# Kernel optimization log

Measured on AMD Instinct MI355X. Metric: run time of the kernel, lower is better.

Reference implementation:

```python
import jax, jax.numpy as jnp
import numpy as np

B, S, D, U = 32, 4096, 512, 128

def setup_inputs() -> dict:
    key = jax.random.key(0)
    k1, k2, k3, k4, k5 = jax.random.split(key, 5)
    query = jax.random.normal(k1, (B, D), dtype=jnp.float32)
    values = jax.random.normal(k2, (B, S, D), dtype=jnp.float32)
    s = 1.0 / np.sqrt(D)
    W1 = jax.random.normal(k3, (D, U), dtype=jnp.float32) * s
    W2 = jax.random.normal(k4, (D, U), dtype=jnp.float32) * s
    V = jax.random.normal(k5, (U, 1), dtype=jnp.float32) * (1.0 / np.sqrt(U))
    b1 = jnp.zeros((U,), dtype=jnp.float32)
    b2 = jnp.zeros((U,), dtype=jnp.float32)
    bv = jnp.zeros((1,), dtype=jnp.float32)
    return {"query": query, "values": values, "W1": W1, "b1": b1,
            "W2": W2, "b2": b2, "V": V, "bv": bv}

def reference(query, values, W1, b1, W2, b2, V, bv):
    # query: [B, D] -> [B, 1, U]; values: [B, S, D] -> [B, S, U]
    q_proj = (query @ W1 + b1)[:, None, :]                  # [B, 1, U]
    v_proj = jnp.einsum('bsd,du->bsu', values, W2) + b2      # [B, S, U]
    score = jnp.tanh(q_proj + v_proj) @ V + bv               # [B, S, 1]
    attention_weights = jax.nn.softmax(score, axis=1)        # [B, S, 1]
    context_vector = jnp.sum(attention_weights * values, axis=1)  # [B, D]
    return context_vector, attention_weights
```

## Files before the change

### kernel.cpp

```cpp
#include <hip/hip_runtime.h>
#include <math.h>

#define NB 32
#define NS 4096
#define ND 512
#define NU 128
#define RR 32
#define ASTR 520
#define BSTR 40

typedef __bf16 bf16x8 __attribute__((ext_vector_type(8)));
typedef unsigned short u16x8 __attribute__((ext_vector_type(8)));
typedef float f32x4 __attribute__((ext_vector_type(4)));

union FragCvt { u16x8 u; bf16x8 b; };

__device__ inline unsigned short f2bf(float x) {
  union { float f; unsigned u; } v; v.f = x;
  return (unsigned short)((v.u + 0x7FFFu + ((v.u >> 16) & 1u)) >> 16);
}
__device__ inline float bf2f(unsigned int bits16) {
  union { unsigned u; float f; } v; v.u = bits16 << 16;
  return v.f;
}

__global__ void prep_qb(const float* __restrict__ q, const float* __restrict__ W1,
                        const float* __restrict__ b1, const float* __restrict__ b2,
                        float* __restrict__ qb) {
  int idx = blockIdx.x * 256 + threadIdx.x;
  int b = idx >> 7, u = idx & 127;
  float s = b1[u] + b2[u];
  const float* qr = q + b * ND;
  for (int d = 0; d < ND; ++d) s += qr[d] * W1[d * NU + u];
  qb[idx] = s;
}

__global__ void prep_w2t(const float* __restrict__ W2, unsigned short* __restrict__ w2t) {
  int idx = blockIdx.x * 256 + threadIdx.x;
  int u = idx >> 9, d = idx & 511;
  w2t[idx] = f2bf(W2[d * NU + u]);
}

__global__ __launch_bounds__(256, 3) void fused_attn(
    const float* __restrict__ values,
    const float* __restrict__ qb,
    const unsigned short* __restrict__ w2t,
    const float* __restrict__ V,
    const float* __restrict__ bvp,
    float* __restrict__ wout,
    float* __restrict__ Cacc,
    float* __restrict__ Lacc)
{
  __shared__ unsigned short Alds[RR * ASTR];
  __shared__ unsigned short Blds[NU * BSTR];
  __shared__ float sbuf[4][16];
  __shared__ float wlds[RR];

  const int tid = threadIdx.x;
  const int b = blockIdx.x >> 7;
  const int chunk = blockIdx.x & 127;
  const int s0 = chunk * RR;

  const float* vbase = values + ((size_t)b * NS + s0) * ND;
  #pragma unroll
  for (int i = 0; i < 16; ++i) {
    int f = tid + 256 * i;
    int row = f >> 7;
    int c4 = f & 127;
    float4 v = *(const float4*)(vbase + row * ND + c4 * 4);
    ushort4 pk;
    pk.x = f2bf(v.x); pk.y = f2bf(v.y); pk.z = f2bf(v.z); pk.w = f2bf(v.w);
    *(ushort4*)(&Alds[row * ASTR + c4 * 4]) = pk;
  }

  const int wave = tid >> 6, lane = tid & 63;
  const int quad = lane >> 4, lidx = lane & 15;
  const int mtile = wave & 1;
  const int nbase = (wave >> 1) * 64;

  f32x4 acc[4] = {{0.f,0.f,0.f,0.f},{0.f,0.f,0.f,0.f},{0.f,0.f,0.f,0.f},{0.f,0.f,0.f,0.f}};

  const int bu = tid >> 1, bh = tid & 1;
  for (int kt = 0; kt < 16; ++kt) {
    __syncthreads();
    {
      const unsigned short* src = w2t + bu * ND + kt * 32 + bh * 16;
      u16x8 p0 = *(const u16x8*)(src);
      u16x8 p1 = *(const u16x8*)(src + 8);
      *(u16x8*)(&Blds[bu * BSTR + bh * 16])     = p0;
      *(u16x8*)(&Blds[bu * BSTR + bh * 16 + 8]) = p1;
    }
    __syncthreads();
    FragCvt af; af.u = *(const u16x8*)(&Alds[(mtile * 16 + lidx) * ASTR + kt * 32 + quad * 8]);
    #pragma unroll
    for (int nt = 0; nt < 4; ++nt) {
      FragCvt bf; bf.u = *(const u16x8*)(&Blds[(nbase + nt * 16 + lidx) * BSTR + quad * 8]);
      acc[nt] = __builtin_amdgcn_mfma_f32_16x16x32_bf16(af.b, bf.b, acc[nt], 0, 0, 0);
    }
  }

  float part[4] = {0.f, 0.f, 0.f, 0.f};
  #pragma unroll
  for (int nt = 0; nt < 4; ++nt) {
    int col = nbase + nt * 16 + lidx;
    float qv = qb[b * NU + col];
    float vv = V[col];
    #pragma unroll
    for (int r = 0; r < 4; ++r) {
      float t = tanhf(acc[nt][r] + qv);
      part[r] += t * vv;
    }
  }
  #pragma unroll
  for (int m = 1; m <= 8; m <<= 1) {
    #pragma unroll
    for (int r = 0; r < 4; ++r) part[r] += __shfl_xor(part[r], m, 64);
  }
  if (lidx == 0) {
    #pragma unroll
    for (int r = 0; r < 4; ++r) sbuf[wave][quad * 4 + r] = part[r];
  }
  __syncthreads();

  if (tid < 32) {
    int mt = tid >> 4, rr = tid & 15;
    float s = sbuf[mt][rr] + sbuf[mt + 2][rr];
    float e = expf(s + *bvp);
    wout[(size_t)b * NS + s0 + tid] = e;
    wlds[tid] = e;
    float es = e;
    #pragma unroll
    for (int m = 1; m <= 16; m <<= 1) es += __shfl_xor(es, m, 64);
    if (tid == 0) atomicAdd(Lacc + b, es);
  }
  __syncthreads();

  int d0 = tid * 2;
  float c0 = 0.f, c1 = 0.f;
  for (int r = 0; r < RR; ++r) {
    float w = wlds[r];
    unsigned int pk = *(const unsigned int*)(&Alds[r * ASTR + d0]);
    c0 += w * bf2f(pk & 0xFFFFu);
    c1 += w * bf2f(pk >> 16);
  }
  atomicAdd(Cacc + b * ND + d0, c0);
  atomicAdd(Cacc + b * ND + d0 + 1, c1);
}

__global__ void finalize(const float* __restrict__ Cacc, const float* __restrict__ Lacc,
                         float* __restrict__ out) {
  int idx = blockIdx.x * 256 + threadIdx.x;
  if (idx < NB * ND) {
    int b = idx >> 9;
    out[idx] = Cacc[idx] / Lacc[b];
  } else {
    int j = idx - NB * ND;
    int b = j >> 12;
    out[idx] = out[idx] / Lacc[b];
  }
}

extern "C" void kernel_launch(void* const* d_in, const int* in_sizes, int n_in,
                              void* d_out, int out_size, void* d_ws, size_t ws_size,
                              hipStream_t stream) {
  const float* query  = (const float*)d_in[0];
  const float* values = (const float*)d_in[1];
  const float* W1     = (const float*)d_in[2];
  const float* b1     = (const float*)d_in[3];
  const float* W2     = (const float*)d_in[4];
  const float* b2     = (const float*)d_in[5];
  const float* V      = (const float*)d_in[6];
  const float* bv     = (const float*)d_in[7];
  float* out = (float*)d_out;

  char* ws = (char*)d_ws;
  float* Cacc = (float*)ws;
  float* Lacc = (float*)(ws + 65536);
  float* qb   = (float*)(ws + 66048);
  unsigned short* w2t = (unsigned short*)(ws + 66048 + 16384);

  hipMemsetAsync(ws, 0, 66048, stream);

  prep_qb <<<16, 256, 0, stream>>>(query, W1, b1, b2, qb);
  prep_w2t<<<256, 256, 0, stream>>>(W2, w2t);
  fused_attn<<<NB * (NS / RR), 256, 0, stream>>>(values, qb, w2t, V, bv,
                                                 out + NB * ND, Cacc, Lacc);
  finalize<<<(NB * ND + NB * NS) / 256, 256, 0, stream>>>(Cacc, Lacc, out);
}
```

Before: 443.5 us.

## Restructure fused attention: direct global fragments, split-K waves, per-chunk context partials

The main kernel now uses 512 threads. Each wave loads its W2 fragments straight from global memory into registers and converts value rows from fp32 to bf16 in registers, so the LDS staging and the per-k-step barriers are gone. The K dimension is split across wave pairs and the partial sums are combined through LDS. The context sum re-reads values in fp32 from global (likely L2-resident) and writes per-chunk partials instead of issuing atomics, and finalize reduces those partials. The two prep kernels are merged into one launch and the memset shrinks. In exchange, values are read twice from memory/cache and the workspace grows to 8 MB of partials.

```diff
diff --git a/kernel.cpp b/kernel.cpp
--- a/kernel.cpp
+++ b/kernel.cpp
@@ -1,4 +1,5 @@
 #include <hip/hip_runtime.h>
+#include <hip/hip_bf16.h>
 #include <math.h>
 
 #define NB 32
@@ -6,125 +7,145 @@
 #define ND 512
 #define NU 128
 #define RR 32
-#define ASTR 520
-#define BSTR 40
+#define NCHUNK (NS / RR)
 
 typedef __bf16 bf16x8 __attribute__((ext_vector_type(8)));
 typedef unsigned short u16x8 __attribute__((ext_vector_type(8)));
 typedef float f32x4 __attribute__((ext_vector_type(4)));
-
 union FragCvt { u16x8 u; bf16x8 b; };
 
 __device__ inline unsigned short f2bf(float x) {
   union { float f; unsigned u; } v; v.f = x;
   return (unsigned short)((v.u + 0x7FFFu + ((v.u >> 16) & 1u)) >> 16);
 }
-__device__ inline float bf2f(unsigned int bits16) {
-  union { unsigned u; float f; } v; v.u = bits16 << 16;
-  return v.f;
-}
-
-__global__ void prep_qb(const float* __restrict__ q, const float* __restrict__ W1,
-                        const float* __restrict__ b1, const float* __restrict__ b2,
-                        float* __restrict__ qb) {
-  int idx = blockIdx.x * 256 + threadIdx.x;
-  int b = idx >> 7, u = idx & 127;
-  float s = b1[u] + b2[u];
-  const float* qr = q + b * ND;
-  for (int d = 0; d < ND; ++d) s += qr[d] * W1[d * NU + u];
-  qb[idx] = s;
-}
-
-__global__ void prep_w2t(const float* __restrict__ W2, unsigned short* __restrict__ w2t) {
-  int idx = blockIdx.x * 256 + threadIdx.x;
-  int u = idx >> 9, d = idx & 511;
-  w2t[idx] = f2bf(W2[d * NU + u]);
-}
-
-__global__ __launch_bounds__(256, 3) void fused_attn(
+
+__device__ inline u16x8 pack8(float4 a, float4 b) {
+  u16x8 r;
+  r[0] = f2bf(a.x); r[1] = f2bf(a.y); r[2] = f2bf(a.z); r[3] = f2bf(a.w);
+  r[4] = f2bf(b.x); r[5] = f2bf(b.y); r[6] = f2bf(b.z); r[7] = f2bf(b.w);
+  return r;
+}
+
+__global__ void prep(const float* __restrict__ q, const float* __restrict__ W1,
+                     const float* __restrict__ b1, const float* __restrict__ b2,
+                     const float* __restrict__ W2,
+                     float* __restrict__ qb, unsigned short* __restrict__ w2t) {
+  if (blockIdx.x < 16) {
+    int idx = blockIdx.x * 256 + threadIdx.x;
+    int b = idx >> 7, u = idx & 127;
+    float s = b1[u] + b2[u];
+    const float* qr = q + b * ND;
+    #pragma unroll 8
+    for (int d = 0; d < ND; ++d) s += qr[d] * W1[d * NU + u];
+    qb[idx] = s;
+  } else {
+    int idx = (blockIdx.x - 16) * 256 + threadIdx.x;
+    int u = idx >> 9, d = idx & 511;
+    w2t[idx] = f2bf(W2[d * NU + u]);
+  }
+}
+
+__global__ __launch_bounds__(512, 4) void fused_attn(
     const float* __restrict__ values,
     const float* __restrict__ qb,
     const unsigned short* __restrict__ w2t,
     const float* __restrict__ V,
     const float* __restrict__ bvp,
     float* __restrict__ wout,
-    float* __restrict__ Cacc,
+    float* __restrict__ Cpart,
     float* __restrict__ Lacc)
 {
-  __shared__ unsigned short Alds[RR * ASTR];
-  __shared__ unsigned short Blds[NU * BSTR];
-  __shared__ float sbuf[4][16];
-  __shared__ float wlds[RR];
+  __shared__ float cbuf[4][16][64];
+  __shared__ float sbuf[4][32];
+  __shared__ float wlds[32];
 
   const int tid = threadIdx.x;
   const int b = blockIdx.x >> 7;
   const int chunk = blockIdx.x & 127;
   const int s0 = chunk * RR;
-
-  const float* vbase = values + ((size_t)b * NS + s0) * ND;
-  #pragma unroll
-  for (int i = 0; i < 16; ++i) {
-    int f = tid + 256 * i;
-    int row = f >> 7;
-    int c4 = f & 127;
-    float4 v = *(const float4*)(vbase + row * ND + c4 * 4);
-    ushort4 pk;
-    pk.x = f2bf(v.x); pk.y = f2bf(v.y); pk.z = f2bf(v.z); pk.w = f2bf(v.w);
-    *(ushort4*)(&Alds[row * ASTR + c4 * 4]) = pk;
-  }
-
   const int wave = tid >> 6, lane = tid & 63;
   const int quad = lane >> 4, lidx = lane & 15;
-  const int mtile = wave & 1;
-  const int nbase = (wave >> 1) * 64;
-
-  f32x4 acc[4] = {{0.f,0.f,0.f,0.f},{0.f,0.f,0.f,0.f},{0.f,0.f,0.f,0.f},{0.f,0.f,0.f,0.f}};
-
-  const int bu = tid >> 1, bh = tid & 1;
-  for (int kt = 0; kt < 16; ++kt) {
-    __syncthreads();
-    {
-      const unsigned short* src = w2t + bu * ND + kt * 32 + bh * 16;
-      u16x8 p0 = *(const u16x8*)(src);
-      u16x8 p1 = *(const u16x8*)(src + 8);
-      *(u16x8*)(&Blds[bu * BSTR + bh * 16])     = p0;
-      *(u16x8*)(&Blds[bu * BSTR + bh * 16 + 8]) = p1;
-    }
-    __syncthreads();
-    FragCvt af; af.u = *(const u16x8*)(&Alds[(mtile * 16 + lidx) * ASTR + kt * 32 + quad * 8]);
-    #pragma unroll
-    for (int nt = 0; nt < 4; ++nt) {
-      FragCvt bf; bf.u = *(const u16x8*)(&Blds[(nbase + nt * 16 + lidx) * BSTR + quad * 8]);
-      acc[nt] = __builtin_amdgcn_mfma_f32_16x16x32_bf16(af.b, bf.b, acc[nt], 0, 0, 0);
-    }
-  }
-
-  float part[4] = {0.f, 0.f, 0.f, 0.f};
+  const int khalf = wave & 1, ng = wave >> 1;
+
+  const float* vbase = values + ((size_t)b * NS + s0) * ND;
+
+  FragCvt bfr[2][8];
   #pragma unroll
-  for (int nt = 0; nt < 4; ++nt) {
-    int col = nbase + nt * 16 + lidx;
-    float qv = qb[b * NU + col];
-    float vv = V[col];
-    #pragma unroll
-    for (int r = 0; r < 4; ++r) {
-      float t = tanhf(acc[nt][r] + qv);
-      part[r] += t * vv;
-    }
-  }
+  for (int nt = 0; nt < 2; ++nt) {
+    const int u = ng * 32 + nt * 16 + lidx;
+    #pragma unroll
+    for (int k8 = 0; k8 < 8; ++k8)
+      bfr[nt][k8].u = *(const u16x8*)(w2t + u * ND + (khalf * 8 + k8) * 32 + quad * 8);
+  }
+
+  f32x4 acc[2][2];
   #pragma unroll
-  for (int m = 1; m <= 8; m <<= 1) {
-    #pragma unroll
-    for (int r = 0; r < 4; ++r) part[r] += __shfl_xor(part[r], m, 64);
-  }
-  if (lidx == 0) {
-    #pragma unroll
-    for (int r = 0; r < 4; ++r) sbuf[wave][quad * 4 + r] = part[r];
+  for (int mt = 0; mt < 2; ++mt)
+    #pragma unroll
+    for (int nt = 0; nt < 2; ++nt)
+      acc[mt][nt] = (f32x4){0.f, 0.f, 0.f, 0.f};
+
+  #pragma unroll
+  for (int k8 = 0; k8 < 8; ++k8) {
+    const int kc = (khalf * 8 + k8) * 32 + quad * 8;
+    #pragma unroll
+    for (int mt = 0; mt < 2; ++mt) {
+      const float* ap = vbase + (mt * 16 + lidx) * ND + kc;
+      float4 a0 = *(const float4*)ap;
+      float4 a1 = *(const float4*)(ap + 4);
+      FragCvt af; af.u = pack8(a0, a1);
+      #pragma unroll
+      for (int nt = 0; nt < 2; ++nt)
+        acc[mt][nt] = __builtin_amdgcn_mfma_f32_16x16x32_bf16(af.b, bfr[nt][k8].b, acc[mt][nt], 0, 0, 0);
+    }
+  }
+
+  if (khalf == 1) {
+    #pragma unroll
+    for (int mt = 0; mt < 2; ++mt)
+      #pragma unroll
+      for (int nt = 0; nt < 2; ++nt)
+        #pragma unroll
+        for (int r = 0; r < 4; ++r)
+          cbuf[ng][mt * 8 + nt * 4 + r][lane] = acc[mt][nt][r];
   }
   __syncthreads();
 
+  if (khalf == 0) {
+    float part[2][4] = {{0.f,0.f,0.f,0.f},{0.f,0.f,0.f,0.f}};
+    #pragma unroll
+    for (int mt = 0; mt < 2; ++mt) {
+      #pragma unroll
+      for (int nt = 0; nt < 2; ++nt) {
+        const int col = ng * 32 + nt * 16 + lidx;
+        const float qv = qb[b * NU + col];
+        const float vv = V[col];
+        #pragma unroll
+        for (int r = 0; r < 4; ++r) {
+          float full = acc[mt][nt][r] + cbuf[ng][mt * 8 + nt * 4 + r][lane];
+          part[mt][r] += tanhf(full + qv) * vv;
+        }
+      }
+    }
+    #pragma unroll
+    for (int m = 1; m <= 8; m <<= 1)
+      #pragma unroll
+      for (int mt = 0; mt < 2; ++mt)
+        #pragma unroll
+        for (int r = 0; r < 4; ++r)
+          part[mt][r] += __shfl_xor(part[mt][r], m, 64);
+    if (lidx == 0) {
+      #pragma unroll
+      for (int mt = 0; mt < 2; ++mt)
+        #pragma unroll
+        for (int r = 0; r < 4; ++r)
+          sbuf[ng][mt * 16 + quad * 4 + r] = part[mt][r];
+    }
+  }
+  __syncthreads();
+
   if (tid < 32) {
-    int mt = tid >> 4, rr = tid & 15;
-    float s = sbuf[mt][rr] + sbuf[mt + 2][rr];
+    float s = sbuf[0][tid] + sbuf[1][tid] + sbuf[2][tid] + sbuf[3][tid];
     float e = expf(s + *bvp);
     wout[(size_t)b * NS + s0 + tid] = e;
     wlds[tid] = e;
@@ -135,24 +156,28 @@
   }
   __syncthreads();
 
-  int d0 = tid * 2;
-  float c0 = 0.f, c1 = 0.f;
-  for (int r = 0; r < RR; ++r) {
-    float w = wlds[r];
-    unsigned int pk = *(const unsigned int*)(&Alds[r * ASTR + d0]);
-    c0 += w * bf2f(pk & 0xFFFFu);
-    c1 += w * bf2f(pk >> 16);
-  }
-  atomicAdd(Cacc + b * ND + d0, c0);
-  atomicAdd(Cacc + b * ND + d0 + 1, c1);
-}
-
-__global__ void finalize(const float* __restrict__ Cacc, const float* __restrict__ Lacc,
+  float c = 0.f;
+  #pragma unroll 8
+  for (int r = 0; r < RR; ++r)
+    c += wlds[r] * vbase[r * ND + tid];
+  Cpart[(size_t)blockIdx.x * ND + tid] = c;
+}
+
+__global__ void finalize(const float* __restrict__ Cpart, const float* __restrict__ Lacc,
                          float* __restrict__ out) {
   int idx = blockIdx.x * 256 + threadIdx.x;
   if (idx < NB * ND) {
-    int b = idx >> 9;
-    out[idx] = Cacc[idx] / Lacc[b];
+    int b = idx >> 9, d = idx & 511;
+    const float* p = Cpart + (size_t)b * NCHUNK * ND + d;
+    float a0 = 0.f, a1 = 0.f, a2 = 0.f, a3 = 0.f;
+    #pragma unroll 4
+    for (int c = 0; c < NCHUNK; c += 4) {
+      a0 += p[(size_t)(c + 0) * ND];
+      a1 += p[(size_t)(c + 1) * ND];
+      a2 += p[(size_t)(c + 2) * ND];
+      a3 += p[(size_t)(c + 3) * ND];
+    }
+    out[idx] = (a0 + a1 + a2 + a3) / Lacc[b];
   } else {
     int j = idx - NB * ND;
     int b = j >> 12;
@@ -174,16 +199,15 @@
   float* out = (float*)d_out;
 
   char* ws = (char*)d_ws;
-  float* Cacc = (float*)ws;
-  float* Lacc = (float*)(ws + 65536);
-  float* qb   = (float*)(ws + 66048);
-  unsigned short* w2t = (unsigned short*)(ws + 66048 + 16384);
-
-  hipMemsetAsync(ws, 0, 66048, stream);
-
-  prep_qb <<<16, 256, 0, stream>>>(query, W1, b1, b2, qb);
-  prep_w2t<<<256, 256, 0, stream>>>(W2, w2t);
-  fused_attn<<<NB * (NS / RR), 256, 0, stream>>>(values, qb, w2t, V, bv,
-                                                 out + NB * ND, Cacc, Lacc);
-  finalize<<<(NB * ND + NB * NS) / 256, 256, 0, stream>>>(Cacc, Lacc, out);
-}
+  float* Cpart = (float*)ws;
+  float* Lacc  = (float*)(ws + 8388608);
+  float* qbuf  = (float*)(ws + 8389120);
+  unsigned short* w2t = (unsigned short*)(ws + 8405504);
+
+  hipMemsetAsync(Lacc, 0, 512, stream);
+
+  prep<<<272, 256, 0, stream>>>(query, W1, b1, b2, W2, qbuf, w2t);
+  fused_attn<<<NB * NCHUNK, 512, 0, stream>>>(values, qbuf, w2t, V, bv,
+                                              out + NB * ND, Cpart, Lacc);
+  finalize<<<576, 256, 0, stream>>>(Cpart, Lacc, out);
+}
```

New measurement: 531.6 us. 19.9% more time.
